# Optimization experiments

Measured on AMD Instinct MI355X. Metric: run time of the kernel, lower is better.

The kernel has to match this reference:

```python
import jax, jax.numpy as jnp
import numpy as np

LN_EPS = 1e-5


def _layernorm(x, gamma, beta):
    mu = jnp.mean(x, axis=-1, keepdims=True)
    var = jnp.mean(jnp.square(x - mu), axis=-1, keepdims=True)
    return (x - mu) * jax.lax.rsqrt(var + LN_EPS) * gamma + beta


def setup_inputs() -> dict:
    key = jax.random.key(0)
    ks = jax.random.split(key, 8)
    B, T, C, H, HS = 8, 2048, 384, 6, 64
    s = C ** -0.5
    return {
        "x": jax.random.normal(ks[0], (B, T, C), jnp.float32),
        "wq": jax.random.normal(ks[1], (H, C, HS), jnp.float32) * s,
        "wk": jax.random.normal(ks[2], (H, C, HS), jnp.float32) * s,
        "wv": jax.random.normal(ks[3], (H, C, HS), jnp.float32) * s,
        "w_proj": jax.random.normal(ks[4], (C, C), jnp.float32) * s,
        "b_proj": jnp.zeros((C,), jnp.float32),
        "w1": jax.random.normal(ks[5], (C, 4 * C), jnp.float32) * s,
        "b1": jnp.zeros((4 * C,), jnp.float32),
        "w2": jax.random.normal(ks[6], (4 * C, C), jnp.float32) * (4 * C) ** -0.5,
        "b2": jnp.zeros((C,), jnp.float32),
        "g1": jnp.ones((C,), jnp.float32),
        "be1": jnp.zeros((C,), jnp.float32),
        "g2": jnp.ones((C,), jnp.float32),
        "be2": jnp.zeros((C,), jnp.float32),
    }


def reference(x, wq, wk, wv, w_proj, b_proj, w1, b1, w2, b2, g1, be1, g2, be2):
    B, T, C = x.shape
    HS = wq.shape[-1]
    # --- multi-head causal self-attention (per-head linear, concat, proj) ---
    q = jnp.einsum("btc,hcd->bhtd", x, wq)
    k = jnp.einsum("btc,hcd->bhtd", x, wk)
    v = jnp.einsum("btc,hcd->bhtd", x, wv)
    scores = jnp.einsum("bhtd,bhsd->bhts", q, k) * (HS ** -0.5)
    causal = jnp.tril(jnp.ones((T, T), bool))
    scores = jnp.where(causal, scores, -jnp.inf)
    att = jax.nn.softmax(scores, axis=-1)  # dropout = identity (eval)
    o = jnp.einsum("bhts,bhsd->bhtd", att, v)
    o = o.transpose(0, 2, 1, 3).reshape(B, T, C)  # concat heads
    sa = o @ w_proj + b_proj
    # --- post-LN residual ---
    x = _layernorm(x + sa, g1, be1)
    # --- feed-forward ---
    ff = jax.nn.relu(x @ w1 + b1) @ w2 + b2
    x = _layernorm(x + ff, g2, be2)
    return x
```

## Files before the change

### kernel.cpp

```cpp
#include <hip/hip_runtime.h>

typedef unsigned short u16;
typedef unsigned int u32;
typedef u16 u16x4 __attribute__((ext_vector_type(4)));
typedef u16 u16x8 __attribute__((ext_vector_type(8)));
typedef u32 u32x4 __attribute__((ext_vector_type(4)));
typedef __bf16 bf16v8 __attribute__((ext_vector_type(8)));
typedef float f32x4 __attribute__((ext_vector_type(4)));
typedef float f32x2 __attribute__((ext_vector_type(2)));

#define DEV __device__ __forceinline__

DEV u16 f2bf(float f) {
  union { float f; u32 u; } v; v.f = f;
  u32 r = v.u + 0x7fffu + ((v.u >> 16) & 1u);
  return (u16)(r >> 16);
}
DEV float bf2f(u16 u) { union { u32 u; float f; } v; v.u = ((u32)u) << 16; return v.f; }
DEV float bfu32lo(u32 w) { union { u32 u; float f; } v; v.u = w << 16; return v.f; }
DEV float bfu32hi(u32 w) { union { u32 u; float f; } v; v.u = w & 0xffff0000u; return v.f; }

DEV u32 cvtpk(float a, float b) {
  u32 d;
  asm("v_cvt_pk_bf16_f32 %0, %1, %2" : "=v"(d) : "v"(a), "v"(b));
  return d;
}

DEV f32x4 mfma16(u16x8 a, u16x8 b, f32x4 c) {
  return __builtin_amdgcn_mfma_f32_16x16x32_bf16(
      __builtin_bit_cast(bf16v8, a), __builtin_bit_cast(bf16v8, b), c, 0, 0, 0);
}

typedef const __attribute__((address_space(1))) void* gas_ptr;
typedef __attribute__((address_space(3))) void* las_ptr;
#define GLOAD16(GP, LP) __builtin_amdgcn_global_load_lds((gas_ptr)(GP), (las_ptr)(LP), 16, 0, 0)

__global__ __launch_bounds__(256) void prep_kernel(
    const float* __restrict__ x, u16* __restrict__ xb,
    const float* __restrict__ wq, const float* __restrict__ wk,
    const float* __restrict__ wv, const float* __restrict__ wproj,
    const float* __restrict__ w1, const float* __restrict__ w2,
    u16* __restrict__ wqkvt, u16* __restrict__ wprojt,
    u16* __restrict__ w1t, u16* __restrict__ w2t) {
  const int bid = blockIdx.x;
  if (bid < 3072) {
    int i = bid * 256 + threadIdx.x;
    const f32x4* p = (const f32x4*)x;
    f32x4 a = p[2 * i], b = p[2 * i + 1];
    u16x8 o;
    #pragma unroll
    for (int j = 0; j < 4; ++j) { o[j] = f2bf(a[j]); o[4 + j] = f2bf(b[j]); }
    *((u16x8*)xb + i) = o;
    return;
  }
  int idx = (bid - 3072) * 256 + threadIdx.x;
  if (idx < 442368) {
    int n = idx / 384, c = idx % 384;
    int which = n / 384;
    int hd = n % 384;
    int h = hd >> 6, d = hd & 63;
    const float* src = (which == 0) ? wq : ((which == 1) ? wk : wv);
    wqkvt[idx] = f2bf(src[((size_t)h * 384 + c) * 64 + d]);
  } else if (idx < 442368 + 147456) {
    int e = idx - 442368;
    int n = e / 384, c = e % 384;
    wprojt[e] = f2bf(wproj[(size_t)c * 384 + n]);
  } else if (idx < 442368 + 147456 + 589824) {
    int e = idx - (442368 + 147456);
    int n = e / 384, c = e % 384;
    w1t[e] = f2bf(w1[(size_t)c * 1536 + n]);
  } else {
    int e = idx - (442368 + 147456 + 589824);
    int n = e / 1536, c = e % 1536;
    w2t[e] = f2bf(w2[(size_t)c * 384 + n]);
  }
}

template <int K, int EPI>
__global__ __launch_bounds__(256) void gemm_kernel(
    const u16* __restrict__ A, const u16* __restrict__ Bt, const int N,
    const float* __restrict__ bias, const u16* __restrict__ resb,
    void* __restrict__ outv, void* __restrict__ outv2) {
  __shared__ u16 sm[24576];
  u16* As = sm;
  u16* Bs = sm + 8192;
  const int t = threadIdx.x;
  const int w = t >> 6, l = t & 63, l15 = l & 15, lg = l >> 4;
  const int wcol = w * 32;
  const int m0 = blockIdx.x * 64, n0 = blockIdx.y * 128;
  const int lr8 = l >> 3;
  const int su = (l & 7) ^ lr8;
  const u16* gA = A + (size_t)(m0 + lr8) * K + su * 8;
  const u16* gB = Bt + (size_t)(n0 + lr8) * K + su * 8;

  f32x4 acc[4][2];
  #pragma unroll
  for (int i = 0; i < 4; ++i)
    #pragma unroll
    for (int j = 0; j < 2; ++j) acc[i][j] = (f32x4){0.f, 0.f, 0.f, 0.f};

  auto stage = [&](int kt, int buf) {
    #pragma unroll
    for (int c = 0; c < 2; ++c)
      GLOAD16(gA + (size_t)(w * 16 + c * 8) * K + kt * 64,
              (char*)As + buf * 8192 + w * 2048 + c * 1024);
    #pragma unroll
    for (int c = 0; c < 4; ++c)
      GLOAD16(gB + (size_t)(w * 32 + c * 8) * K + kt * 64,
              (char*)Bs + buf * 16384 + w * 4096 + c * 1024);
  };

  constexpr int NT = K / 64;
  int cur = 0;
  stage(0, 0);
  #pragma unroll 1
  for (int kt = 0; kt < NT; ++kt) {
    __syncthreads();
    if (kt + 1 < NT) stage(kt + 1, cur ^ 1);
    const u16* Ab = As + cur * 4096;
    const u16* Bb = Bs + cur * 8192;
    u16x8 af[4][2], bfr[2][2];
    #pragma unroll
    for (int i = 0; i < 4; ++i) {
      const int row = i * 16 + l15;
      #pragma unroll
      for (int ks = 0; ks < 2; ++ks)
        af[i][ks] = *(const u16x8*)&Ab[row * 64 + (((4 * ks + lg) ^ (row & 7)) << 3)];
    }
    #pragma unroll
    for (int j = 0; j < 2; ++j) {
      const int row = wcol + j * 16 + l15;
      #pragma unroll
      for (int ks = 0; ks < 2; ++ks)
        bfr[j][ks] = *(const u16x8*)&Bb[row * 64 + (((4 * ks + lg) ^ (row & 7)) << 3)];
    }
    #pragma unroll
    for (int ks = 0; ks < 2; ++ks)
      #pragma unroll
      for (int mi = 0; mi < 4; ++mi)
        #pragma unroll
        for (int ni = 0; ni < 2; ++ni)
          acc[mi][ni] = mfma16(af[mi][ks], bfr[ni][ks], acc[mi][ni]);
    cur ^= 1;
  }

  __syncthreads();
  if (EPI == 0 && n0 >= 768) {
    #pragma unroll
    for (int mi = 0; mi < 4; ++mi)
      #pragma unroll
      for (int ni = 0; ni < 2; ++ni) {
        const int rowg = m0 + mi * 16 + lg * 4;
        const int hd = n0 + wcol + ni * 16 + l15 - 768;
        u16x4 pv;
        #pragma unroll
        for (int r = 0; r < 4; ++r) pv[r] = f2bf(acc[mi][ni][r]);
        *(u16x4*)((u16*)outv2 + (size_t)((rowg >> 11) * 6 + (hd >> 6)) * 131072 +
                  (size_t)(hd & 63) * 2048 + (rowg & 2047)) = pv;
      }
    return;
  }
  u16* Wl = sm + w * 4096;
  #pragma unroll
  for (int mi = 0; mi < 4; ++mi)
    #pragma unroll
    for (int ni = 0; ni < 2; ++ni) {
      float b_ = 0.f;
      if constexpr (EPI != 0) b_ = bias[n0 + wcol + ni * 16 + l15];
      #pragma unroll
      for (int r = 0; r < 4; ++r) {
        float v = acc[mi][ni][r] + b_;
        if constexpr (EPI == 2) v = fmaxf(v, 0.f);
        Wl[(mi * 16 + lg * 4 + r) * 40 + ni * 16 + l15] = f2bf(v);
      }
    }
  asm volatile("s_waitcnt lgkmcnt(0)" ::: "memory");
  __builtin_amdgcn_sched_barrier(0);
  const int rcol = (l & 3) * 8;
  #pragma unroll
  for (int p = 0; p < 4; ++p) {
    const int row = (l >> 2) + 16 * p;
    u16x8 cv = *(const u16x8*)&Wl[row * 40 + rcol];
    const size_t off = (size_t)(m0 + row) * N + n0 + wcol + rcol;
    if constexpr (EPI == 1) {
      u16x8 rv = *(const u16x8*)&resb[off];
      u32 ov[4];
      #pragma unroll
      for (int j = 0; j < 4; ++j)
        ov[j] = cvtpk(bf2f(cv[2 * j]) + bf2f(rv[2 * j]),
                      bf2f(cv[2 * j + 1]) + bf2f(rv[2 * j + 1]));
      *(u32x4*)((u16*)outv + off) = (u32x4){ov[0], ov[1], ov[2], ov[3]};
    } else {
      *(u16x8*)((u16*)outv + off) = cv;
    }
  }
}

__global__ __launch_bounds__(256, 5) void attn_kernel(const u16* __restrict__ qk,
                                                      const u16* __restrict__ vt,
                                                      u16* __restrict__ o,
                                                      float* __restrict__ part) {
  __shared__ __align__(16) char smem[32768];

  const int t = threadIdx.x;
  const int w = t >> 6, l = t & 63, l15 = l & 15, lg = l >> 4;
  const int idx = blockIdx.x;
  const int hl = idx % 48;
  const int g = idx / 48;
  int qt, k0, k1, e = 0;
  bool heavy;
  if (g < 32) {
    heavy = true; e = g;
    qt = 31 - (g >> 1);
    const int kmid = (qt + 1) >> 1;
    if (g & 1) { k0 = kmid; k1 = qt + 1; } else { k0 = 0; k1 = kmid; }
  } else {
    heavy = false; qt = 47 - g; k0 = 0; k1 = qt + 1;
  }
  const int b = hl / 6, head = hl % 6;
  const float SC = 0.125f * 1.44269504f;
  const float FM = 17.312340f;

  u16x8 qf[2];
  {
    const u16* qp = qk + (size_t)b * 2048 * 768 +
                    (size_t)(qt * 64 + w * 16 + l15) * 768 + head * 64 + lg * 8;
    qf[0] = *(const u16x8*)qp;
    qf[1] = *(const u16x8*)(qp + 32);
  }
  u16x8 ones;
  #pragma unroll
  for (int j = 0; j < 8; ++j) ones[j] = 0x3F80;

  f32x4 Oa[4];
  f32x4 Osum = (f32x4){0.f, 0.f, 0.f, 0.f};
  #pragma unroll
  for (int i = 0; i < 4; ++i) Oa[i] = (f32x4){0.f, 0.f, 0.f, 0.f};

  const int su16 = ((l & 7) ^ (l >> 3)) << 4;
  const char* kg0 = (const char*)qk + (size_t)b * 2048 * 1536 +
                    (size_t)(w * 8 + (l >> 3)) * 1536 + (size_t)(384 + head * 64) * 2 + su16;
  const char* vg0 = (const char*)vt + (size_t)(b * 6 + head) * 262144 +
                    (size_t)(w * 8 + (l >> 3)) * 4096 + su16;

  auto stage = [&](int kt, int bufsel) {
    const char* kg = kg0 + (size_t)kt * 98304;
    const char* vg = vg0 + (size_t)kt * 128;
    char* kl = smem + bufsel * 8192 + w * 1024;
    char* vl = smem + 16384 + bufsel * 8192 + w * 1024;
    GLOAD16(kg, kl);
    GLOAD16(kg + 49152, kl + 4096);
    GLOAD16(vg, vl);
    GLOAD16(vg + 131072, vl + 4096);
  };

  auto compute = [&](int bufoff, bool diag) {
    f32x4 sa[4];
    __builtin_amdgcn_s_setprio(1);
    #pragma unroll
    for (int st = 0; st < 4; ++st) {
      sa[st] = (f32x4){0.f, 0.f, 0.f, 0.f};
      const int sr = st * 16 + l15;
      #pragma unroll
      for (int ks = 0; ks < 2; ++ks) {
        u16x8 kf = *(const u16x8*)(smem + bufoff + sr * 128 +
                                   (((ks * 4 + lg) ^ (sr & 7)) << 4));
        sa[st] = mfma16(kf, qf[ks], sa[st]);
      }
    }
    __builtin_amdgcn_s_setprio(0);
    if (diag) {
      #pragma unroll
      for (int st = 0; st < 4; ++st)
        #pragma unroll
        for (int r = 0; r < 4; ++r)
          if (st * 16 + lg * 4 + r > w * 16 + l15) sa[st][r] = -3.0e38f;
    }
    u32 pk2[4][2];
    #pragma unroll
    for (int st = 0; st < 4; ++st) {
      float e0 = exp2f(sa[st][0] * SC - FM);
      float e1 = exp2f(sa[st][1] * SC - FM);
      float e2 = exp2f(sa[st][2] * SC - FM);
      float e3 = exp2f(sa[st][3] * SC - FM);
      pk2[st][0] = cvtpk(e0, e1);
      pk2[st][1] = cvtpk(e2, e3);
    }
    #pragma unroll
    for (int ks = 0; ks < 2; ++ks) {
      u32 wds[4];
      #pragma unroll
      for (int wd = 0; wd < 4; ++wd) {
        int src = ((2 * (lg & 1) + (wd >> 1)) << 4) | l15;
        u32 c0 = (u32)__shfl((int)pk2[2 * ks][wd & 1], src);
        u32 c1 = (u32)__shfl((int)pk2[2 * ks + 1][wd & 1], src);
        wds[wd] = (lg & 2) ? c1 : c0;
      }
      u16x8 pf = __builtin_bit_cast(u16x8, (u32x4){wds[0], wds[1], wds[2], wds[3]});
      __builtin_amdgcn_s_setprio(1);
      #pragma unroll
      for (int dt = 0; dt < 4; ++dt) {
        const int dd = dt * 16 + l15;
        u16x8 vf = *(const u16x8*)(smem + 16384 + bufoff + dd * 128 +
                                   (((ks * 4 + lg) ^ (dd & 7)) << 4));
        Oa[dt] = mfma16(pf, vf, Oa[dt]);
      }
      Osum = mfma16(pf, ones, Osum);
      __builtin_amdgcn_s_setprio(0);
    }
  };

  int cur = 0;
  stage(k0, 0);
  #pragma unroll 1
  for (int kt = k0; kt < k1; ++kt) {
    __syncthreads();
    if (kt + 1 < k1) stage(kt + 1, cur ^ 1);
    compute(cur * 8192, kt == qt);
    cur ^= 1;
  }

  if (!heavy) {
    float inv[4];
    #pragma unroll
    for (int r = 0; r < 4; ++r) inv[r] = 1.0f / Osum[r];
    #pragma unroll
    for (int dt = 0; dt < 4; ++dt)
      #pragma unroll
      for (int r = 0; r < 4; ++r) {
        size_t row = (size_t)b * 2048 + qt * 64 + w * 16 + lg * 4 + r;
        o[row * 384 + head * 64 + dt * 16 + l15] = f2bf(Oa[dt][r] * inv[r]);
      }
  } else {
    float* slot = part + (size_t)(hl * 32 + e) * 4224;
    if (l15 == 0) {
      #pragma unroll
      for (int r = 0; r < 4; ++r) slot[w * 16 + lg * 4 + r] = Osum[r];
    }
    #pragma unroll
    for (int dt = 0; dt < 4; ++dt)
      #pragma unroll
      for (int r = 0; r < 4; ++r)
        slot[128 + (w * 16 + lg * 4 + r) * 64 + dt * 16 + l15] = Oa[dt][r];
  }
}

__global__ __launch_bounds__(256) void attn_combine_kernel(const float* __restrict__ part,
                                                           u16* __restrict__ o) {
  const int idx = blockIdx.x;
  const int hl = idx % 48;
  const int qt = 31 - idx / 48;
  const int e0 = (31 - qt) * 2;
  const float* s0 = part + (size_t)(hl * 32 + e0) * 4224;
  const float* s1 = s0 + 4224;
  const int t = threadIdx.x;
  const int row = t >> 2, c0 = (t & 3) * 16;
  const float inv = 1.0f / (s0[row] + s1[row]);
  const int b = hl / 6, head = hl % 6;
  const f32x4* a0 = (const f32x4*)(s0 + 128 + row * 64 + c0);
  const f32x4* a1 = (const f32x4*)(s1 + 128 + row * 64 + c0);
  u32 wv[8];
  #pragma unroll
  for (int j = 0; j < 4; ++j) {
    f32x4 va = a0[j], vb = a1[j];
    float y0 = (va[0] + vb[0]) * inv;
    float y1 = (va[1] + vb[1]) * inv;
    float y2 = (va[2] + vb[2]) * inv;
    float y3 = (va[3] + vb[3]) * inv;
    wv[2 * j] = cvtpk(y0, y1);
    wv[2 * j + 1] = cvtpk(y2, y3);
  }
  u16* op = o + ((size_t)(b * 2048 + qt * 64 + row)) * 384 + head * 64 + c0;
  *(u32x4*)op = (u32x4){wv[0], wv[1], wv[2], wv[3]};
  *(u32x4*)(op + 8) = (u32x4){wv[4], wv[5], wv[6], wv[7]};
}

template <int IN_BF16, int OUT_BF16>
__global__ __launch_bounds__(256) void ln_kernel(const void* __restrict__ inv,
                                                 const float* __restrict__ g,
                                                 const float* __restrict__ be,
                                                 void* __restrict__ outv) {
  const int row = blockIdx.x * 4 + (threadIdx.x >> 6);
  const int lane = threadIdx.x & 63;
  float v[6];
  if constexpr (IN_BF16) {
    const u16* pb = (const u16*)inv + (size_t)row * 384 + lane * 6;
    u32 w0 = *(const u32*)pb, w1 = *(const u32*)(pb + 2), w2 = *(const u32*)(pb + 4);
    v[0] = bfu32lo(w0); v[1] = bfu32hi(w0);
    v[2] = bfu32lo(w1); v[3] = bfu32hi(w1);
    v[4] = bfu32lo(w2); v[5] = bfu32hi(w2);
  } else {
    const float* p = (const float*)inv + (size_t)row * 384 + lane * 6;
    const f32x2* p2 = (const f32x2*)p;
    f32x2 a0 = p2[0], a1 = p2[1], a2 = p2[2];
    v[0] = a0[0]; v[1] = a0[1]; v[2] = a1[0]; v[3] = a1[1]; v[4] = a2[0]; v[5] = a2[1];
  }
  float s = v[0] + v[1] + v[2] + v[3] + v[4] + v[5];
  #pragma unroll
  for (int m = 1; m < 64; m <<= 1) s += __shfl_xor(s, m, 64);
  const float mu = s * (1.0f / 384.0f);
  float d2 = 0.f;
  #pragma unroll
  for (int j = 0; j < 6; ++j) { float d = v[j] - mu; d2 += d * d; }
  #pragma unroll
  for (int m = 1; m < 64; m <<= 1) d2 += __shfl_xor(d2, m, 64);
  const float rstd = rsqrtf(d2 * (1.0f / 384.0f) + 1e-5f);
  const int c = lane * 6;
  float y[6];
  #pragma unroll
  for (int j = 0; j < 6; ++j) y[j] = (v[j] - mu) * rstd * g[c + j] + be[c + j];
  if constexpr (OUT_BF16) {
    u32* ob = (u32*)((u16*)outv + (size_t)row * 384 + c);
    #pragma unroll
    for (int j = 0; j < 3; ++j) ob[j] = cvtpk(y[2 * j], y[2 * j + 1]);
  } else {
    float* of = (float*)outv + (size_t)row * 384 + c;
    f32x2* o2 = (f32x2*)of;
    #pragma unroll
    for (int j = 0; j < 3; ++j) o2[j] = (f32x2){y[2 * j], y[2 * j + 1]};
  }
}

extern "C" void kernel_launch(void* const* d_in, const int* in_sizes, int n_in,
                              void* d_out, int out_size, void* d_ws, size_t ws_size,
                              hipStream_t stream) {
  const float* x     = (const float*)d_in[0];
  const float* wq    = (const float*)d_in[1];
  const float* wk    = (const float*)d_in[2];
  const float* wv    = (const float*)d_in[3];
  const float* wproj = (const float*)d_in[4];
  const float* bproj = (const float*)d_in[5];
  const float* w1    = (const float*)d_in[6];
  const float* b1    = (const float*)d_in[7];
  const float* w2    = (const float*)d_in[8];
  const float* b2    = (const float*)d_in[9];
  const float* g1    = (const float*)d_in[10];
  const float* be1   = (const float*)d_in[11];
  const float* g2    = (const float*)d_in[12];
  const float* be2   = (const float*)d_in[13];

  char* ws = (char*)d_ws;
  u16*   xb    = (u16*)(ws + 0);
  u16*   qk    = (u16*)(ws + 12582912);
  u16*   vt    = (u16*)(ws + 37748736);
  u16*   obuf  = (u16*)(ws + 50331648);
  float* part  = (float*)(ws + 62914560);
  u16*   x1b   = (u16*)(ws + 88080384);
  u16*   wqkvt = (u16*)(ws + 100663296);
  u16*   wprjt = (u16*)(ws + 101548032);
  u16*   w1t   = (u16*)(ws + 101842944);
  u16*   w2t   = (u16*)(ws + 103022592);
  u16*   r1b   = (u16*)(ws + 62914560);
  u16*   h1    = qk;
  u16*   r2b   = xb;

  prep_kernel<<<9984, 256, 0, stream>>>(x, xb, wq, wk, wv, wproj, w1, w2,
                                        wqkvt, wprjt, w1t, w2t);
  gemm_kernel<384, 0><<<dim3(256, 9), 256, 0, stream>>>(xb, wqkvt, 768, nullptr, nullptr, qk, vt);
  attn_kernel<<<2304, 256, 0, stream>>>(qk, vt, obuf, part);
  attn_combine_kernel<<<768, 256, 0, stream>>>(part, obuf);
  gemm_kernel<384, 1><<<dim3(256, 3), 256, 0, stream>>>(obuf, wprjt, 384, bproj, xb, r1b, nullptr);
  ln_kernel<1, 1><<<4096, 256, 0, stream>>>(r1b, g1, be1, x1b);
  gemm_kernel<384, 2><<<dim3(256, 12), 256, 0, stream>>>(x1b, w1t, 1536, b1, nullptr, h1, nullptr);
  gemm_kernel<1536, 1><<<dim3(256, 3), 256, 0, stream>>>(h1, w2t, 384, b2, x1b, r2b, nullptr);
  ln_kernel<1, 0><<<4096, 256, 0, stream>>>(r2b, g2, be2, d_out);
}
```

Measured before the change: 191.4 us.

## Process two query tiles per attention block to reuse staged K/V tiles

Each attention workgroup now handles a 128-row query strip, two 64-row groups, instead of one 64-row tile. Every K/V tile staged into shared memory feeds both groups' MFMAs, which halves K/V global and LDS traffic per query row and halves the grid. The heavy/light split and the partial-result layout and combine indexing are reworked to match. The cost is doubled accumulator registers, with launch bounds lowered from 5 to 4 blocks per SIMD, and fewer, larger blocks that may load-balance worse.

```diff
diff --git a/kernel.cpp b/kernel.cpp
--- a/kernel.cpp
+++ b/kernel.cpp
@@ -196,7 +196,7 @@
   }
 }
 
-__global__ __launch_bounds__(256, 5) void attn_kernel(const u16* __restrict__ qk,
+__global__ __launch_bounds__(256, 4) void attn_kernel(const u16* __restrict__ qk,
                                                       const u16* __restrict__ vt,
                                                       u16* __restrict__ o,
                                                       float* __restrict__ part) {
@@ -205,37 +205,47 @@
   const int t = threadIdx.x;
   const int w = t >> 6, l = t & 63, l15 = l & 15, lg = l >> 4;
   const int idx = blockIdx.x;
-  const int hl = idx % 48;
-  const int g = idx / 48;
-  int qt, k0, k1, e = 0;
+  int qs, k0, k1, e = 0, hl;
   bool heavy;
-  if (g < 32) {
-    heavy = true; e = g;
-    qt = 31 - (g >> 1);
-    const int kmid = (qt + 1) >> 1;
-    if (g & 1) { k0 = kmid; k1 = qt + 1; } else { k0 = 0; k1 = kmid; }
+  if (idx < 768) {
+    heavy = true;
+    const int j = idx / 48;
+    hl = idx % 48;
+    qs = 15 - (j >> 1);
+    e = j & 1;
+    const int kmid = qs + 1;
+    if (e) { k0 = kmid; k1 = 2 * qs + 2; } else { k0 = 0; k1 = kmid; }
   } else {
-    heavy = false; qt = 47 - g; k0 = 0; k1 = qt + 1;
+    heavy = false;
+    const int j = (idx - 768) / 48;
+    hl = (idx - 768) % 48;
+    qs = 7 - j;
+    k0 = 0; k1 = 2 * qs + 2;
   }
   const int b = hl / 6, head = hl % 6;
   const float SC = 0.125f * 1.44269504f;
   const float FM = 17.312340f;
 
-  u16x8 qf[2];
-  {
+  u16x8 qf[2][2];
+  #pragma unroll
+  for (int g = 0; g < 2; ++g) {
     const u16* qp = qk + (size_t)b * 2048 * 768 +
-                    (size_t)(qt * 64 + w * 16 + l15) * 768 + head * 64 + lg * 8;
-    qf[0] = *(const u16x8*)qp;
-    qf[1] = *(const u16x8*)(qp + 32);
+                    (size_t)(qs * 128 + g * 64 + w * 16 + l15) * 768 + head * 64 + lg * 8;
+    qf[g][0] = *(const u16x8*)qp;
+    qf[g][1] = *(const u16x8*)(qp + 32);
   }
   u16x8 ones;
   #pragma unroll
   for (int j = 0; j < 8; ++j) ones[j] = 0x3F80;
 
-  f32x4 Oa[4];
-  f32x4 Osum = (f32x4){0.f, 0.f, 0.f, 0.f};
-  #pragma unroll
-  for (int i = 0; i < 4; ++i) Oa[i] = (f32x4){0.f, 0.f, 0.f, 0.f};
+  f32x4 Oa[2][4];
+  f32x4 Osum[2];
+  #pragma unroll
+  for (int g = 0; g < 2; ++g) {
+    Osum[g] = (f32x4){0.f, 0.f, 0.f, 0.f};
+    #pragma unroll
+    for (int i = 0; i < 4; ++i) Oa[g][i] = (f32x4){0.f, 0.f, 0.f, 0.f};
+  }
 
   const int su16 = ((l & 7) ^ (l >> 3)) << 4;
   const char* kg0 = (const char*)qk + (size_t)b * 2048 * 1536 +
@@ -254,58 +264,71 @@
     GLOAD16(vg + 131072, vl + 4096);
   };
 
-  auto compute = [&](int bufoff, bool diag) {
-    f32x4 sa[4];
-    __builtin_amdgcn_s_setprio(1);
+  auto buildpf = [&](u32 (&pk2)[4][2], int ks) -> u16x8 {
+    u32 wds[4];
+    #pragma unroll
+    for (int wd = 0; wd < 4; ++wd) {
+      int src = ((2 * (lg & 1) + (wd >> 1)) << 4) | l15;
+      u32 c0 = (u32)__shfl((int)pk2[2 * ks][wd & 1], src);
+      u32 c1 = (u32)__shfl((int)pk2[2 * ks + 1][wd & 1], src);
+      wds[wd] = (lg & 2) ? c1 : c0;
+    }
+    return __builtin_bit_cast(u16x8, (u32x4){wds[0], wds[1], wds[2], wds[3]});
+  };
+
+  auto compute = [&](int bufoff, int kt) {
+    const bool act0 = (kt <= 2 * qs);
+    const bool d0 = (kt == 2 * qs);
+    const bool d1 = (kt == 2 * qs + 1);
+    u32 pkA[4][2], pkB[4][2];
     #pragma unroll
     for (int st = 0; st < 4; ++st) {
-      sa[st] = (f32x4){0.f, 0.f, 0.f, 0.f};
       const int sr = st * 16 + l15;
-      #pragma unroll
-      for (int ks = 0; ks < 2; ++ks) {
-        u16x8 kf = *(const u16x8*)(smem + bufoff + sr * 128 +
-                                   (((ks * 4 + lg) ^ (sr & 7)) << 4));
-        sa[st] = mfma16(kf, qf[ks], sa[st]);
-      }
-    }
-    __builtin_amdgcn_s_setprio(0);
-    if (diag) {
-      #pragma unroll
-      for (int st = 0; st < 4; ++st)
+      u16x8 kf0 = *(const u16x8*)(smem + bufoff + sr * 128 + ((lg ^ (sr & 7)) << 4));
+      u16x8 kf1 = *(const u16x8*)(smem + bufoff + sr * 128 + (((4 + lg) ^ (sr & 7)) << 4));
+      __builtin_amdgcn_s_setprio(1);
+      f32x4 s1v = (f32x4){0.f, 0.f, 0.f, 0.f};
+      s1v = mfma16(kf0, qf[1][0], s1v);
+      s1v = mfma16(kf1, qf[1][1], s1v);
+      __builtin_amdgcn_s_setprio(0);
+      if (d1) {
         #pragma unroll
         for (int r = 0; r < 4; ++r)
-          if (st * 16 + lg * 4 + r > w * 16 + l15) sa[st][r] = -3.0e38f;
-    }
-    u32 pk2[4][2];
-    #pragma unroll
-    for (int st = 0; st < 4; ++st) {
-      float e0 = exp2f(sa[st][0] * SC - FM);
-      float e1 = exp2f(sa[st][1] * SC - FM);
-      float e2 = exp2f(sa[st][2] * SC - FM);
-      float e3 = exp2f(sa[st][3] * SC - FM);
-      pk2[st][0] = cvtpk(e0, e1);
-      pk2[st][1] = cvtpk(e2, e3);
+          if (st * 16 + lg * 4 + r > w * 16 + l15) s1v[r] = -3.0e38f;
+      }
+      pkB[st][0] = cvtpk(exp2f(s1v[0] * SC - FM), exp2f(s1v[1] * SC - FM));
+      pkB[st][1] = cvtpk(exp2f(s1v[2] * SC - FM), exp2f(s1v[3] * SC - FM));
+      if (act0) {
+        __builtin_amdgcn_s_setprio(1);
+        f32x4 s0v = (f32x4){0.f, 0.f, 0.f, 0.f};
+        s0v = mfma16(kf0, qf[0][0], s0v);
+        s0v = mfma16(kf1, qf[0][1], s0v);
+        __builtin_amdgcn_s_setprio(0);
+        if (d0) {
+          #pragma unroll
+          for (int r = 0; r < 4; ++r)
+            if (st * 16 + lg * 4 + r > w * 16 + l15) s0v[r] = -3.0e38f;
+        }
+        pkA[st][0] = cvtpk(exp2f(s0v[0] * SC - FM), exp2f(s0v[1] * SC - FM));
+        pkA[st][1] = cvtpk(exp2f(s0v[2] * SC - FM), exp2f(s0v[3] * SC - FM));
+      }
     }
     #pragma unroll
     for (int ks = 0; ks < 2; ++ks) {
-      u32 wds[4];
-      #pragma unroll
-      for (int wd = 0; wd < 4; ++wd) {
-        int src = ((2 * (lg & 1) + (wd >> 1)) << 4) | l15;
-        u32 c0 = (u32)__shfl((int)pk2[2 * ks][wd & 1], src);
-        u32 c1 = (u32)__shfl((int)pk2[2 * ks + 1][wd & 1], src);
-        wds[wd] = (lg & 2) ? c1 : c0;
-      }
-      u16x8 pf = __builtin_bit_cast(u16x8, (u32x4){wds[0], wds[1], wds[2], wds[3]});
+      u16x8 pfB = buildpf(pkB, ks);
+      u16x8 pfA;
+      if (act0) pfA = buildpf(pkA, ks);
       __builtin_amdgcn_s_setprio(1);
       #pragma unroll
       for (int dt = 0; dt < 4; ++dt) {
         const int dd = dt * 16 + l15;
         u16x8 vf = *(const u16x8*)(smem + 16384 + bufoff + dd * 128 +
                                    (((ks * 4 + lg) ^ (dd & 7)) << 4));
-        Oa[dt] = mfma16(pf, vf, Oa[dt]);
+        Oa[1][dt] = mfma16(pfB, vf, Oa[1][dt]);
+        if (act0) Oa[0][dt] = mfma16(pfA, vf, Oa[0][dt]);
       }
-      Osum = mfma16(pf, ones, Osum);
+      Osum[1] = mfma16(pfB, ones, Osum[1]);
+      if (act0) Osum[0] = mfma16(pfA, ones, Osum[0]);
       __builtin_amdgcn_s_setprio(0);
     }
   };
@@ -316,61 +339,71 @@
   for (int kt = k0; kt < k1; ++kt) {
     __syncthreads();
     if (kt + 1 < k1) stage(kt + 1, cur ^ 1);
-    compute(cur * 8192, kt == qt);
+    compute(cur * 8192, kt);
     cur ^= 1;
   }
 
   if (!heavy) {
-    float inv[4];
-    #pragma unroll
-    for (int r = 0; r < 4; ++r) inv[r] = 1.0f / Osum[r];
-    #pragma unroll
-    for (int dt = 0; dt < 4; ++dt)
-      #pragma unroll
-      for (int r = 0; r < 4; ++r) {
-        size_t row = (size_t)b * 2048 + qt * 64 + w * 16 + lg * 4 + r;
-        o[row * 384 + head * 64 + dt * 16 + l15] = f2bf(Oa[dt][r] * inv[r]);
-      }
+    #pragma unroll
+    for (int g = 0; g < 2; ++g) {
+      float inv[4];
+      #pragma unroll
+      for (int r = 0; r < 4; ++r) inv[r] = 1.0f / Osum[g][r];
+      #pragma unroll
+      for (int dt = 0; dt < 4; ++dt)
+        #pragma unroll
+        for (int r = 0; r < 4; ++r) {
+          size_t row = (size_t)b * 2048 + qs * 128 + g * 64 + w * 16 + lg * 4 + r;
+          o[row * 384 + head * 64 + dt * 16 + l15] = f2bf(Oa[g][dt][r] * inv[r]);
+        }
+    }
   } else {
-    float* slot = part + (size_t)(hl * 32 + e) * 4224;
+    float* slot = part + (size_t)(((hl * 8 + (qs - 8)) * 2) + e) * 8320;
     if (l15 == 0) {
       #pragma unroll
-      for (int r = 0; r < 4; ++r) slot[w * 16 + lg * 4 + r] = Osum[r];
-    }
-    #pragma unroll
-    for (int dt = 0; dt < 4; ++dt)
-      #pragma unroll
-      for (int r = 0; r < 4; ++r)
-        slot[128 + (w * 16 + lg * 4 + r) * 64 + dt * 16 + l15] = Oa[dt][r];
+      for (int g = 0; g < 2; ++g)
+        #pragma unroll
+        for (int r = 0; r < 4; ++r)
+          slot[g * 64 + w * 16 + lg * 4 + r] = Osum[g][r];
+    }
+    #pragma unroll
+    for (int g = 0; g < 2; ++g)
+      #pragma unroll
+      for (int dt = 0; dt < 4; ++dt)
+        #pragma unroll
+        for (int r = 0; r < 4; ++r)
+          slot[128 + (size_t)(g * 64 + w * 16 + lg * 4 + r) * 64 + dt * 16 + l15] =
+              Oa[g][dt][r];
   }
 }
 
 __global__ __launch_bounds__(256) void attn_combine_kernel(const float* __restrict__ part,
                                                            u16* __restrict__ o) {
   const int idx = blockIdx.x;
+  const int j = idx / 48;
   const int hl = idx % 48;
-  const int qt = 31 - idx / 48;
-  const int e0 = (31 - qt) * 2;
-  const float* s0 = part + (size_t)(hl * 32 + e0) * 4224;
-  const float* s1 = s0 + 4224;
+  const int qs = 8 + (j >> 1);
+  const int rh = j & 1;
+  const float* s0 = part + (size_t)((hl * 8 + (qs - 8)) * 2) * 8320;
+  const float* s1 = s0 + 8320;
   const int t = threadIdx.x;
-  const int row = t >> 2, c0 = (t & 3) * 16;
+  const int row = rh * 64 + (t >> 2), c0 = (t & 3) * 16;
   const float inv = 1.0f / (s0[row] + s1[row]);
   const int b = hl / 6, head = hl % 6;
-  const f32x4* a0 = (const f32x4*)(s0 + 128 + row * 64 + c0);
-  const f32x4* a1 = (const f32x4*)(s1 + 128 + row * 64 + c0);
+  const f32x4* a0 = (const f32x4*)(s0 + 128 + (size_t)row * 64 + c0);
+  const f32x4* a1 = (const f32x4*)(s1 + 128 + (size_t)row * 64 + c0);
   u32 wv[8];
   #pragma unroll
-  for (int j = 0; j < 4; ++j) {
-    f32x4 va = a0[j], vb = a1[j];
+  for (int j2 = 0; j2 < 4; ++j2) {
+    f32x4 va = a0[j2], vb = a1[j2];
     float y0 = (va[0] + vb[0]) * inv;
     float y1 = (va[1] + vb[1]) * inv;
     float y2 = (va[2] + vb[2]) * inv;
     float y3 = (va[3] + vb[3]) * inv;
-    wv[2 * j] = cvtpk(y0, y1);
-    wv[2 * j + 1] = cvtpk(y2, y3);
-  }
-  u16* op = o + ((size_t)(b * 2048 + qt * 64 + row)) * 384 + head * 64 + c0;
+    wv[2 * j2] = cvtpk(y0, y1);
+    wv[2 * j2 + 1] = cvtpk(y2, y3);
+  }
+  u16* op = o + ((size_t)(b * 2048 + qs * 128 + row)) * 384 + head * 64 + c0;
   *(u32x4*)op = (u32x4){wv[0], wv[1], wv[2], wv[3]};
   *(u32x4*)(op + 8) = (u32x4){wv[4], wv[5], wv[6], wv[7]};
 }
@@ -457,7 +490,7 @@
   prep_kernel<<<9984, 256, 0, stream>>>(x, xb, wq, wk, wv, wproj, w1, w2,
                                         wqkvt, wprjt, w1t, w2t);
   gemm_kernel<384, 0><<<dim3(256, 9), 256, 0, stream>>>(xb, wqkvt, 768, nullptr, nullptr, qk, vt);
-  attn_kernel<<<2304, 256, 0, stream>>>(qk, vt, obuf, part);
+  attn_kernel<<<1152, 256, 0, stream>>>(qk, vt, obuf, part);
   attn_combine_kernel<<<768, 256, 0, stream>>>(part, obuf);
   gemm_kernel<384, 1><<<dim3(256, 3), 256, 0, stream>>>(obuf, wprjt, 384, bproj, xb, r1b, nullptr);
   ln_kernel<1, 1><<<4096, 256, 0, stream>>>(r1b, g1, be1, x1b);
```

Measured after the change: 198.3 us. 1.04x slower.

## Load attention K/V fragments directly from global memory instead of LDS staging

Applied to the files above, without the earlier changes.

Removes the double-buffered shared-memory staging of K and V tiles in the attention kernel. Each wave now reads its K and V MFMA fragments straight from global memory into registers every key tile, and the __syncthreads barrier and LDS swizzle go away. This drops the barrier cost and LDS traffic. In exchange, each of the four waves loads the same K/V tile redundantly, with strided, less coalesced access and no prefetch overlap. The occupancy hint in launch bounds is also removed.

```diff
diff --git a/kernel.cpp b/kernel.cpp
--- a/kernel.cpp
+++ b/kernel.cpp
@@ -196,12 +196,10 @@
   }
 }
 
-__global__ __launch_bounds__(256, 5) void attn_kernel(const u16* __restrict__ qk,
-                                                      const u16* __restrict__ vt,
-                                                      u16* __restrict__ o,
-                                                      float* __restrict__ part) {
-  __shared__ __align__(16) char smem[32768];
-
+__global__ __launch_bounds__(256) void attn_kernel(const u16* __restrict__ qk,
+                                                   const u16* __restrict__ vt,
+                                                   u16* __restrict__ o,
+                                                   float* __restrict__ part) {
   const int t = threadIdx.x;
   const int w = t >> 6, l = t & 63, l15 = l & 15, lg = l >> 4;
   const int idx = blockIdx.x;
@@ -237,39 +235,35 @@
   #pragma unroll
   for (int i = 0; i < 4; ++i) Oa[i] = (f32x4){0.f, 0.f, 0.f, 0.f};
 
-  const int su16 = ((l & 7) ^ (l >> 3)) << 4;
-  const char* kg0 = (const char*)qk + (size_t)b * 2048 * 1536 +
-                    (size_t)(w * 8 + (l >> 3)) * 1536 + (size_t)(384 + head * 64) * 2 + su16;
-  const char* vg0 = (const char*)vt + (size_t)(b * 6 + head) * 262144 +
-                    (size_t)(w * 8 + (l >> 3)) * 4096 + su16;
-
-  auto stage = [&](int kt, int bufsel) {
-    const char* kg = kg0 + (size_t)kt * 98304;
-    const char* vg = vg0 + (size_t)kt * 128;
-    char* kl = smem + bufsel * 8192 + w * 1024;
-    char* vl = smem + 16384 + bufsel * 8192 + w * 1024;
-    GLOAD16(kg, kl);
-    GLOAD16(kg + 49152, kl + 4096);
-    GLOAD16(vg, vl);
-    GLOAD16(vg + 131072, vl + 4096);
-  };
-
-  auto compute = [&](int bufoff, bool diag) {
+  const u16* kb = qk + (size_t)b * 2048 * 768 + (size_t)l15 * 768 + 384 + head * 64 + lg * 8;
+  const u16* vb = vt + (size_t)(b * 6 + head) * 131072 + (size_t)l15 * 2048 + lg * 8;
+
+  #pragma unroll 1
+  for (int kt = k0; kt < k1; ++kt) {
+    const u16* kbt = kb + (size_t)kt * 64 * 768;
+    const u16* vbt = vb + kt * 64;
+    u16x8 vfr[2][4];
+    #pragma unroll
+    for (int ks = 0; ks < 2; ++ks)
+      #pragma unroll
+      for (int dt = 0; dt < 4; ++dt)
+        vfr[ks][dt] = *(const u16x8*)&vbt[dt * 32768 + ks * 32];
+    u16x8 kfr[4][2];
+    #pragma unroll
+    for (int st = 0; st < 4; ++st)
+      #pragma unroll
+      for (int ks = 0; ks < 2; ++ks)
+        kfr[st][ks] = *(const u16x8*)&kbt[st * 16 * 768 + ks * 32];
     f32x4 sa[4];
     __builtin_amdgcn_s_setprio(1);
     #pragma unroll
     for (int st = 0; st < 4; ++st) {
       sa[st] = (f32x4){0.f, 0.f, 0.f, 0.f};
-      const int sr = st * 16 + l15;
-      #pragma unroll
-      for (int ks = 0; ks < 2; ++ks) {
-        u16x8 kf = *(const u16x8*)(smem + bufoff + sr * 128 +
-                                   (((ks * 4 + lg) ^ (sr & 7)) << 4));
-        sa[st] = mfma16(kf, qf[ks], sa[st]);
-      }
+      sa[st] = mfma16(kfr[st][0], qf[0], sa[st]);
+      sa[st] = mfma16(kfr[st][1], qf[1], sa[st]);
     }
     __builtin_amdgcn_s_setprio(0);
-    if (diag) {
+    if (kt == qt) {
       #pragma unroll
       for (int st = 0; st < 4; ++st)
         #pragma unroll
@@ -299,25 +293,11 @@
       u16x8 pf = __builtin_bit_cast(u16x8, (u32x4){wds[0], wds[1], wds[2], wds[3]});
       __builtin_amdgcn_s_setprio(1);
       #pragma unroll
-      for (int dt = 0; dt < 4; ++dt) {
-        const int dd = dt * 16 + l15;
-        u16x8 vf = *(const u16x8*)(smem + 16384 + bufoff + dd * 128 +
-                                   (((ks * 4 + lg) ^ (dd & 7)) << 4));
-        Oa[dt] = mfma16(pf, vf, Oa[dt]);
-      }
+      for (int dt = 0; dt < 4; ++dt)
+        Oa[dt] = mfma16(pf, vfr[ks][dt], Oa[dt]);
       Osum = mfma16(pf, ones, Osum);
       __builtin_amdgcn_s_setprio(0);
     }
-  };
-
-  int cur = 0;
-  stage(k0, 0);
-  #pragma unroll 1
-  for (int kt = k0; kt < k1; ++kt) {
-    __syncthreads();
-    if (kt + 1 < k1) stage(kt + 1, cur ^ 1);
-    compute(cur * 8192, kt == qt);
-    cur ^= 1;
   }
 
   if (!heavy) {
```

After: 318.5 us. 66.4% more time.
